# Performance work log

Hardware: AMD Instinct MI355X
Metric: run time of the kernel (lower is better)

## Reference

```python
import jax, jax.numpy as jnp
import numpy as np

IN_FEATURES = 512
OUT_FEATURES = 256
N = 2048

def setup_inputs() -> dict:
    key = jax.random.key(0)
    k1, k2, k3 = jax.random.split(key, 3)
    x = jax.random.normal(k1, (N, IN_FEATURES), dtype=jnp.float32)
    # kaiming_uniform_(a=sqrt(5)) -> uniform(-b, b) with b = sqrt(6/((1+5)*fan_in)) = 1/sqrt(fan_in)
    bound_w = 1.0 / np.sqrt(IN_FEATURES)
    weight = jax.random.uniform(k2, (OUT_FEATURES, IN_FEATURES), dtype=jnp.float32,
                                minval=-bound_w, maxval=bound_w)
    bound_b = 1.0 / np.sqrt(IN_FEATURES)
    bias = jax.random.uniform(k3, (OUT_FEATURES,), dtype=jnp.float32,
                              minval=-bound_b, maxval=bound_b)
    return {"x": x, "weight": weight, "bias": bias}

def reference(x, weight, bias):
    # MAM fully-connected (beta == 0 path):
    # prod[n, k, j] = x[n, k] * weight[j, k]
    # C[n, j] = max_k prod[n,k,j] + min_k prod[n,k,j] + bias[j]
    prod = x[:, :, None] * weight.T[None, :, :]   # [N, in, out]
    C = jnp.max(prod, axis=1) + jnp.min(prod, axis=1) + bias[None, :]
    return C
```

## Files before the change

kernel.cpp:

```cpp
#include <hip/hip_runtime.h>
#include <math.h>

#define N_ 2048
#define K_ 512
#define J_ 256
#define TN 64
#define TJ 32
#define BK 256
#define RP 260

typedef __attribute__((address_space(3))) float       lds_f;
typedef const __attribute__((address_space(1))) float glb_f;

__global__ __launch_bounds__(256) void mam_fused(
    const float* __restrict__ x, const float* __restrict__ w,
    const float* __restrict__ bias, float* __restrict__ out)
{
    __shared__ __align__(16) float xs[TN * RP];
    __shared__ __align__(16) float wsh[TJ * RP];

    const int t    = threadIdx.x;
    const int lane = t & 63;
    const int wid  = t >> 6;
    const int j0   = blockIdx.x * TJ;
    const int n0   = blockIdx.y * TN;
    const int tx   = t & 15;
    const int ty   = t >> 4;

    float mx[4][2], mn[4][2];
#pragma unroll
    for (int i = 0; i < 4; ++i)
#pragma unroll
        for (int j = 0; j < 2; ++j) {
            mx[i][j] = -__builtin_inff();
            mn[i][j] =  __builtin_inff();
        }

    for (int kc = 0; kc < K_; kc += BK) {
#pragma unroll
        for (int r = 0; r < 16; ++r) {
            const int row = wid * 16 + r;
            __builtin_amdgcn_global_load_lds(
                (glb_f*)(x + (size_t)(n0 + row) * K_ + kc + lane * 4),
                (lds_f*)(xs + row * RP), 16, 0, 0);
        }
#pragma unroll
        for (int r = 0; r < 8; ++r) {
            const int row = wid * 8 + r;
            __builtin_amdgcn_global_load_lds(
                (glb_f*)(w + (size_t)(j0 + row) * K_ + kc + lane * 4),
                (lds_f*)(wsh + row * RP), 16, 0, 0);
        }
        __syncthreads();

#pragma unroll 4
        for (int kk = 0; kk < BK; kk += 4) {
            float4 xv[4], wq[2];
#pragma unroll
            for (int i = 0; i < 4; ++i)
                xv[i] = *(const float4*)&xs[(ty * 4 + i) * RP + kk];
#pragma unroll
            for (int j = 0; j < 2; ++j)
                wq[j] = *(const float4*)&wsh[(tx * 2 + j) * RP + kk];
#pragma unroll
            for (int i = 0; i < 4; ++i) {
                const float xa[4] = {xv[i].x, xv[i].y, xv[i].z, xv[i].w};
#pragma unroll
                for (int j = 0; j < 2; ++j) {
                    const float wa[4] = {wq[j].x, wq[j].y, wq[j].z, wq[j].w};
#pragma unroll
                    for (int q = 0; q < 4; ++q) {
                        const float p = xa[q] * wa[q];
                        mx[i][j] = fmaxf(mx[i][j], p);
                        mn[i][j] = fminf(mn[i][j], p);
                    }
                }
            }
        }
        __syncthreads();
    }

    const float2 bi = *(const float2*)&bias[j0 + tx * 2];
#pragma unroll
    for (int i = 0; i < 4; ++i) {
        float2 o;
        o.x = mx[i][0] + mn[i][0] + bi.x;
        o.y = mx[i][1] + mn[i][1] + bi.y;
        *(float2*)&out[(size_t)(n0 + ty * 4 + i) * J_ + j0 + tx * 2] = o;
    }
}

extern "C" void kernel_launch(void* const* d_in, const int* in_sizes, int n_in,
                              void* d_out, int out_size, void* d_ws, size_t ws_size,
                              hipStream_t stream) {
    const float* x    = (const float*)d_in[0];
    const float* w    = (const float*)d_in[1];
    const float* bias = (const float*)d_in[2];
    float* out = (float*)d_out;

    dim3 grid(J_ / TJ, N_ / TN);
    mam_fused<<<grid, 256, 0, stream>>>(x, w, bias, out);
}
```

Before: 83.20 us.

## Rewrite MAM kernel with per-lane rows, wave-uniform weight loads, double-buffered LDS, max3/min3

Restructures the kernel so each lane owns one x row and each wave handles four output columns. Weight values come straight from global memory at wave-uniform addresses, so they can become scalar loads, and only x is staged through a double-buffered LDS pipeline over four K chunks. It also fuses the max/min reductions with inline v_max3/v_min3 asm and remaps block IDs, presumably to improve XCD/L2 locality. Each block now computes fewer outputs (64x16), which lowers per-block reuse of the staged x tile.

After: 86.47 us. +3.9%, slower.

```diff
diff --git a/kernel.cpp b/kernel.cpp
--- a/kernel.cpp
+++ b/kernel.cpp
@@ -4,90 +4,93 @@
 #define N_ 2048
 #define K_ 512
 #define J_ 256
-#define TN 64
-#define TJ 32
-#define BK 256
-#define RP 260
+#define BK 128
+#define NR 64
+#define NPAIR 32
+#define PP 260
 
 typedef __attribute__((address_space(3))) float       lds_f;
 typedef const __attribute__((address_space(1))) float glb_f;
 
-__global__ __launch_bounds__(256) void mam_fused(
+#define MAX3(acc, a, b) asm("v_max3_f32 %0, %0, %1, %2" : "+v"(acc) : "v"(a), "v"(b))
+#define MIN3(acc, a, b) asm("v_min3_f32 %0, %0, %1, %2" : "+v"(acc) : "v"(a), "v"(b))
+
+__global__ __launch_bounds__(256) void mam_fused2(
     const float* __restrict__ x, const float* __restrict__ w,
     const float* __restrict__ bias, float* __restrict__ out)
 {
-    __shared__ __align__(16) float xs[TN * RP];
-    __shared__ __align__(16) float wsh[TJ * RP];
+    __shared__ __align__(16) float xs[2][NPAIR * PP];
 
     const int t    = threadIdx.x;
     const int lane = t & 63;
-    const int wid  = t >> 6;
-    const int j0   = blockIdx.x * TJ;
-    const int n0   = blockIdx.y * TN;
-    const int tx   = t & 15;
-    const int ty   = t >> 4;
+    const int wid  = __builtin_amdgcn_readfirstlane(t >> 6);
 
-    float mx[4][2], mn[4][2];
+    const int wg0 = (int)blockIdx.x;
+    const int wg  = (wg0 & 7) * 64 + (wg0 >> 3);
+    const int bx  = wg & 15;
+    const int by  = wg >> 4;
+
+    const int n0  = by * NR;
+    const int j0w = bx * 16 + wid * 4;
+
+    const int sub = lane >> 5;
+    const int kl  = (lane & 31) * 4;
+
+    const int xoff = (lane >> 1) * PP + (lane & 1) * BK;
+
+    float mx[4], mn[4];
 #pragma unroll
-    for (int i = 0; i < 4; ++i)
-#pragma unroll
-        for (int j = 0; j < 2; ++j) {
-            mx[i][j] = -__builtin_inff();
-            mn[i][j] =  __builtin_inff();
-        }
+    for (int j = 0; j < 4; ++j) { mx[j] = -__builtin_inff(); mn[j] = __builtin_inff(); }
 
-    for (int kc = 0; kc < K_; kc += BK) {
-#pragma unroll
-        for (int r = 0; r < 16; ++r) {
-            const int row = wid * 16 + r;
-            __builtin_amdgcn_global_load_lds(
-                (glb_f*)(x + (size_t)(n0 + row) * K_ + kc + lane * 4),
-                (lds_f*)(xs + row * RP), 16, 0, 0);
-        }
-#pragma unroll
-        for (int r = 0; r < 8; ++r) {
-            const int row = wid * 8 + r;
-            __builtin_amdgcn_global_load_lds(
-                (glb_f*)(w + (size_t)(j0 + row) * K_ + kc + lane * 4),
-                (lds_f*)(wsh + row * RP), 16, 0, 0);
-        }
-        __syncthreads();
-
-#pragma unroll 4
-        for (int kk = 0; kk < BK; kk += 4) {
-            float4 xv[4], wq[2];
-#pragma unroll
-            for (int i = 0; i < 4; ++i)
-                xv[i] = *(const float4*)&xs[(ty * 4 + i) * RP + kk];
-#pragma unroll
-            for (int j = 0; j < 2; ++j)
-                wq[j] = *(const float4*)&wsh[(tx * 2 + j) * RP + kk];
-#pragma unroll
-            for (int i = 0; i < 4; ++i) {
-                const float xa[4] = {xv[i].x, xv[i].y, xv[i].z, xv[i].w};
-#pragma unroll
-                for (int j = 0; j < 2; ++j) {
-                    const float wa[4] = {wq[j].x, wq[j].y, wq[j].z, wq[j].w};
-#pragma unroll
-                    for (int q = 0; q < 4; ++q) {
-                        const float p = xa[q] * wa[q];
-                        mx[i][j] = fmaxf(mx[i][j], p);
-                        mn[i][j] = fminf(mn[i][j], p);
-                    }
-                }
-            }
-        }
-        __syncthreads();
+#define STAGE(buf, kc)                                                            \
+    {                                                                             \
+        _Pragma("unroll")                                                         \
+        for (int p = 0; p < 8; ++p) {                                             \
+            const int pair = wid * 8 + p;                                         \
+            __builtin_amdgcn_global_load_lds(                                     \
+                (glb_f*)(x + (size_t)(n0 + pair * 2 + sub) * K_ + (kc) + kl),     \
+                (lds_f*)(&xs[buf][pair * PP]), 16, 0, 0);                         \
+        }                                                                         \
     }
 
-    const float2 bi = *(const float2*)&bias[j0 + tx * 2];
-#pragma unroll
-    for (int i = 0; i < 4; ++i) {
-        float2 o;
-        o.x = mx[i][0] + mn[i][0] + bi.x;
-        o.y = mx[i][1] + mn[i][1] + bi.y;
-        *(float2*)&out[(size_t)(n0 + ty * 4 + i) * J_ + j0 + tx * 2] = o;
+#define CHUNK(buf, kc)                                                            \
+    {                                                                             \
+        const float* xr = &xs[buf][xoff];                                         \
+        const float* wr = w + (size_t)j0w * K_ + (kc);                            \
+        _Pragma("unroll 8")                                                       \
+        for (int kk = 0; kk < BK; kk += 4) {                                      \
+            const float4 xv = *(const float4*)(xr + kk);                          \
+            _Pragma("unroll")                                                     \
+            for (int j = 0; j < 4; ++j) {                                         \
+                const float4 wv = *(const float4*)(wr + (size_t)j * K_ + kk);     \
+                const float p0 = xv.x * wv.x, p1 = xv.y * wv.y;                   \
+                const float p2 = xv.z * wv.z, p3 = xv.w * wv.w;                   \
+                MAX3(mx[j], p0, p1); MAX3(mx[j], p2, p3);                         \
+                MIN3(mn[j], p0, p1); MIN3(mn[j], p2, p3);                         \
+            }                                                                     \
+        }                                                                         \
     }
+
+    STAGE(0, 0);
+    __syncthreads();
+    STAGE(1, BK);        CHUNK(0, 0);
+    __syncthreads();
+    STAGE(0, 2 * BK);    CHUNK(1, BK);
+    __syncthreads();
+    STAGE(1, 3 * BK);    CHUNK(0, 2 * BK);
+    __syncthreads();
+                         CHUNK(1, 3 * BK);
+
+    const float4 bi = *(const float4*)&bias[j0w];
+    float4 o;
+    o.x = mx[0] + mn[0] + bi.x;
+    o.y = mx[1] + mn[1] + bi.y;
+    o.z = mx[2] + mn[2] + bi.z;
+    o.w = mx[3] + mn[3] + bi.w;
+    *(float4*)&out[(size_t)(n0 + lane) * J_ + j0w] = o;
+
+#undef STAGE
+#undef CHUNK
 }
 
 extern "C" void kernel_launch(void* const* d_in, const int* in_sizes, int n_in,
@@ -98,6 +101,6 @@
     const float* bias = (const float*)d_in[2];
     float* out = (float*)d_out;
 
-    dim3 grid(J_ / TJ, N_ / TN);
-    mam_fused<<<grid, 256, 0, stream>>>(x, w, bias, out);
+    dim3 grid(512);
+    mam_fused2<<<grid, 256, 0, stream>>>(x, w, bias, out);
 }
```

## Rewrite MAM kernel with register-resident weights, scalar x loads, and max3/min3

Applied to the files above, without the earlier changes.

Replaces the LDS-tiled kernel with one where each lane holds a 64-wide K-slice of one weight row in registers. Each wave splits K into eight chunks and broadcasts x rows through scalar loads (s_load_dwordx16). It folds products with v_max3/v_min3 inline asm, then combines the partial max/min across waves through LDS. Block indices are remapped for locality. This removes most LDS traffic and halves the compare instruction count, at the cost of high register pressure, serialized scalar-load waits, and a cross-wave reduction step.

Measured after the change: 73.90 us. 11.2% less time.

```diff
diff --git a/kernel.cpp b/kernel.cpp
--- a/kernel.cpp
+++ b/kernel.cpp
@@ -4,89 +4,87 @@
 #define N_ 2048
 #define K_ 512
 #define J_ 256
-#define TN 64
-#define TJ 32
-#define BK 256
-#define RP 260
+#define KC 64
+#define NPW 16
 
-typedef __attribute__((address_space(3))) float       lds_f;
-typedef const __attribute__((address_space(1))) float glb_f;
+typedef float f32x16 __attribute__((ext_vector_type(16)));
 
-__global__ __launch_bounds__(256) void mam_fused(
+#define MAX3(acc, a, b) asm("v_max3_f32 %0, %0, %1, %2" : "+v"(acc) : "v"(a), "v"(b))
+#define MIN3(acc, a, b) asm("v_min3_f32 %0, %0, %1, %2" : "+v"(acc) : "v"(a), "v"(b))
+
+__global__ __launch_bounds__(512, 4) void mam_fused5(
     const float* __restrict__ x, const float* __restrict__ w,
     const float* __restrict__ bias, float* __restrict__ out)
 {
-    __shared__ __align__(16) float xs[TN * RP];
-    __shared__ __align__(16) float wsh[TJ * RP];
+    __shared__ float cmb[8][NPW][128];
 
     const int t    = threadIdx.x;
     const int lane = t & 63;
-    const int wid  = t >> 6;
-    const int j0   = blockIdx.x * TJ;
-    const int n0   = blockIdx.y * TN;
-    const int tx   = t & 15;
-    const int ty   = t >> 4;
+    const int kc   = __builtin_amdgcn_readfirstlane(t >> 6);
 
-    float mx[4][2], mn[4][2];
+    const int wg0 = (int)blockIdx.x;
+    const int wg  = (wg0 & 7) * 64 + (wg0 >> 3);
+    const int jb  = wg & 3;
+    const int ng  = wg >> 2;
+
+    const int j   = jb * 64 + lane;
+    const int n0  = ng * NPW;
+
+    float4 wreg[16];
+    {
+        const float4* wp = (const float4*)(w + (size_t)j * K_ + kc * KC);
 #pragma unroll
-    for (int i = 0; i < 4; ++i)
-#pragma unroll
-        for (int j = 0; j < 2; ++j) {
-            mx[i][j] = -__builtin_inff();
-            mn[i][j] =  __builtin_inff();
-        }
-
-    for (int kc = 0; kc < K_; kc += BK) {
-#pragma unroll
-        for (int r = 0; r < 16; ++r) {
-            const int row = wid * 16 + r;
-            __builtin_amdgcn_global_load_lds(
-                (glb_f*)(x + (size_t)(n0 + row) * K_ + kc + lane * 4),
-                (lds_f*)(xs + row * RP), 16, 0, 0);
-        }
-#pragma unroll
-        for (int r = 0; r < 8; ++r) {
-            const int row = wid * 8 + r;
-            __builtin_amdgcn_global_load_lds(
-                (glb_f*)(w + (size_t)(j0 + row) * K_ + kc + lane * 4),
-                (lds_f*)(wsh + row * RP), 16, 0, 0);
-        }
-        __syncthreads();
-
-#pragma unroll 4
-        for (int kk = 0; kk < BK; kk += 4) {
-            float4 xv[4], wq[2];
-#pragma unroll
-            for (int i = 0; i < 4; ++i)
-                xv[i] = *(const float4*)&xs[(ty * 4 + i) * RP + kk];
-#pragma unroll
-            for (int j = 0; j < 2; ++j)
-                wq[j] = *(const float4*)&wsh[(tx * 2 + j) * RP + kk];
-#pragma unroll
-            for (int i = 0; i < 4; ++i) {
-                const float xa[4] = {xv[i].x, xv[i].y, xv[i].z, xv[i].w};
-#pragma unroll
-                for (int j = 0; j < 2; ++j) {
-                    const float wa[4] = {wq[j].x, wq[j].y, wq[j].z, wq[j].w};
-#pragma unroll
-                    for (int q = 0; q < 4; ++q) {
-                        const float p = xa[q] * wa[q];
-                        mx[i][j] = fmaxf(mx[i][j], p);
-                        mn[i][j] = fminf(mn[i][j], p);
-                    }
-                }
-            }
-        }
-        __syncthreads();
+        for (int i = 0; i < 16; ++i) wreg[i] = wp[i];
     }
 
-    const float2 bi = *(const float2*)&bias[j0 + tx * 2];
+    const float* xb = x + (size_t)n0 * K_ + kc * KC;
+
+    float mxv[NPW], mnv[NPW];
 #pragma unroll
-    for (int i = 0; i < 4; ++i) {
-        float2 o;
-        o.x = mx[i][0] + mn[i][0] + bi.x;
-        o.y = mx[i][1] + mn[i][1] + bi.y;
-        *(float2*)&out[(size_t)(n0 + ty * 4 + i) * J_ + j0 + tx * 2] = o;
+    for (int n = 0; n < NPW; ++n) { mxv[n] = -__builtin_inff(); mnv[n] = __builtin_inff(); }
+
+#pragma unroll
+    for (int n = 0; n < NPW; ++n) {
+        f32x16 xv[4];
+        asm volatile(
+            "s_load_dwordx16 %0, %4, %5\n\t"
+            "s_load_dwordx16 %1, %4, %6\n\t"
+            "s_load_dwordx16 %2, %4, %7\n\t"
+            "s_load_dwordx16 %3, %4, %8\n\t"
+            "s_waitcnt lgkmcnt(0)"
+            : "=&s"(xv[0]), "=&s"(xv[1]), "=&s"(xv[2]), "=&s"(xv[3])
+            : "s"(xb), "i"(n * 2048 + 0), "i"(n * 2048 + 64),
+              "i"(n * 2048 + 128), "i"(n * 2048 + 192));
+#pragma unroll
+        for (int i = 0; i < 16; ++i) {
+            const float p0 = wreg[i].x * xv[i >> 2][(i & 3) * 4 + 0];
+            const float p1 = wreg[i].y * xv[i >> 2][(i & 3) * 4 + 1];
+            const float p2 = wreg[i].z * xv[i >> 2][(i & 3) * 4 + 2];
+            const float p3 = wreg[i].w * xv[i >> 2][(i & 3) * 4 + 3];
+            MAX3(mxv[n], p0, p1); MAX3(mxv[n], p2, p3);
+            MIN3(mnv[n], p0, p1); MIN3(mnv[n], p2, p3);
+        }
+    }
+
+#pragma unroll
+    for (int n = 0; n < NPW; ++n) {
+        cmb[kc][n][lane]      = mxv[n];
+        cmb[kc][n][64 + lane] = mnv[n];
+    }
+    __syncthreads();
+
+    const float bj = bias[j];
+#pragma unroll
+    for (int u = 0; u < 2; ++u) {
+        const int n = kc * 2 + u;
+        float a = cmb[0][n][lane];
+        float b = cmb[0][n][64 + lane];
+#pragma unroll
+        for (int c = 1; c < 8; ++c) {
+            a = fmaxf(a, cmb[c][n][lane]);
+            b = fminf(b, cmb[c][n][64 + lane]);
+        }
+        out[(size_t)(n0 + n) * J_ + j] = a + b + bj;
     }
 }
 
@@ -98,6 +96,6 @@
     const float* bias = (const float*)d_in[2];
     float* out = (float*)d_out;
 
-    dim3 grid(J_ / TJ, N_ / TN);
-    mam_fused<<<grid, 256, 0, stream>>>(x, w, bias, out);
+    dim3 grid(512);
+    mam_fused5<<<grid, 512, 0, stream>>>(x, w, bias, out);
 }
```
